# Kernel optimization log

Hardware: AMD Instinct MI355X
Metric: run time of the kernel (lower is better)

Reference implementation:

```python
import jax, jax.numpy as jnp
import numpy as np
from jax import lax

WINDOW_SIZE = 11
SIGMA = 1.5
MAX_VAL = 1.0
C1 = (0.01 * MAX_VAL) ** 2
C2 = (0.03 * MAX_VAL) ** 2
PAD = (WINDOW_SIZE - 1) // 2


def _gaussian_kernel2d(ksize: int, sigma: float) -> jnp.ndarray:
    x = jnp.arange(ksize, dtype=jnp.float32) - ksize // 2
    g = jnp.exp(-(x ** 2) / (2.0 * sigma ** 2))
    g = g / jnp.sum(g)
    return jnp.outer(g, g)  # [k, k]


def _filter2d(x: jnp.ndarray, kernel2d: jnp.ndarray) -> jnp.ndarray:
    # depthwise conv: x [B,C,H,W], kernel repeated per channel -> [C,1,k,k]
    c = x.shape[1]
    k = jnp.broadcast_to(kernel2d[None, None], (c, 1, WINDOW_SIZE, WINDOW_SIZE)).astype(x.dtype)
    return lax.conv_general_dilated(
        x, k,
        window_strides=(1, 1),
        padding=((PAD, PAD), (PAD, PAD)),
        dimension_numbers=("NCHW", "OIHW", "NCHW"),
        feature_group_count=c,
    )


def setup_inputs() -> dict:
    key = jax.random.key(0)
    k1, k2 = jax.random.split(key)
    img1 = jax.random.uniform(k1, (16, 3, 512, 512), dtype=jnp.float32)
    img2 = jax.random.uniform(k2, (16, 3, 512, 512), dtype=jnp.float32)
    return {"img1": img1, "img2": img2}


def reference(img1, img2):
    kernel = _gaussian_kernel2d(WINDOW_SIZE, SIGMA)
    mu1 = _filter2d(img1, kernel)
    mu2 = _filter2d(img2, kernel)
    mu1_sq = mu1 * mu1
    mu2_sq = mu2 * mu2
    mu1_mu2 = mu1 * mu2
    sigma1_sq = _filter2d(img1 * img1, kernel) - mu1_sq
    sigma2_sq = _filter2d(img2 * img2, kernel) - mu2_sq
    sigma12 = _filter2d(img1 * img2, kernel) - mu1_mu2
    ssim_map = ((2.0 * mu1_mu2 + C1) * (2.0 * sigma12 + C2)) / (
        (mu1_sq + mu2_sq + C1) * (sigma1_sq + sigma2_sq + C2)
    )
    loss = jnp.clip(1.0 - ssim_map, 0.0, 1.0) / 2.0
    return jnp.mean(loss)  # reduction='mean'
```

## Files before the change

### kernel.cpp

```cpp
#include <hip/hip_runtime.h>


#define BATCH  16
#define CHAN   3
#define H_     512
#define W_     512
#define HW     (H_ * W_)
#define CH_H   32
#define NSTEP  (CH_H + 10)
#define NPIX   ((long)BATCH*CHAN*H_*W_)

#define GW0 0.0010284f
#define GW1 0.0075988f
#define GW2 0.0360008f
#define GW3 0.1093554f
#define GW4 0.2130056f
#define GW5 0.2660117f

typedef float v2  __attribute__((ext_vector_type(2)));
typedef float v4f __attribute__((ext_vector_type(4)));

__device__ __forceinline__ float wg(int k) {
    return (k == 0 || k == 10) ? GW0
         : (k == 1 || k == 9)  ? GW1
         : (k == 2 || k == 8)  ? GW2
         : (k == 3 || k == 7)  ? GW3
         : (k == 4 || k == 6)  ? GW4 : GW5;
}

__device__ __forceinline__ v2 pfma(v2 a, v2 b, v2 c) {
#if __has_builtin(__builtin_elementwise_fma)
    return __builtin_elementwise_fma(a, b, c);
#else
    v2 r; r.x = fmaf(a.x, b.x, c.x); r.y = fmaf(a.y, b.y, c.y); return r;
#endif
}
__device__ __forceinline__ v2 psfma(float s, v2 b, v2 c) {
    v2 sv; sv.x = s; sv.y = s;
    return pfma(sv, b, c);
}

__device__ __forceinline__ float ssim_retire(float mu1, float mu2,
                                             float x11, float x22, float x12) {
    const float c1 = 1.0e-4f;
    const float c2 = 9.0e-4f;
    float mu1s = mu1 * mu1;
    float mu2s = mu2 * mu2;
    float m12  = mu1 * mu2;
    float num  = (2.0f * m12 + c1) * (2.0f * (x12 - m12) + c2);
    float den  = (mu1s + mu2s + c1) * ((x11 - mu1s) + (x22 - mu2s) + c2);
#if __has_builtin(__builtin_amdgcn_rcpf)
    float l = 1.0f - num * __builtin_amdgcn_rcpf(den);
#else
    float l = 1.0f - num / den;
#endif
    return fminf(fmaxf(l, 0.0f), 1.0f);
}

#define DECL(i) v2 P##i = {0.f, 0.f}, Q##i = {0.f, 0.f}; float E##i = 0.f
#define ACCI(i) do { const float wj_ = wg(10 - (i));             \
    P##i = psfma(wj_, hmm, P##i);                                \
    Q##i = psfma(wj_, hss, Q##i);                                \
    E##i = fmaf(wj_, hm12, E##i); } while (0)
#define SHIFT(i, j) P##i = P##j; Q##i = Q##j; E##i = E##j

__global__ __launch_bounds__(256) void ssim_kernel(const float* __restrict__ img1,
                                                   const float* __restrict__ img2,
                                                   float* __restrict__ out) {
    __shared__ __align__(16) v2 sp[4][2][80];
    __shared__ float wsum[4];

    const int tid  = threadIdx.x;
    const int lane = tid & 63;
    const int wv   = tid >> 6;

    const int wid   = blockIdx.x * 4 + wv;
    const int plane = wid >> 7;
    const int rem   = wid & 127;
    const int strip = rem & 7;
    const int chunk = rem >> 3;
    const int y0 = chunk * CH_H;
    const int c0 = strip * 64;

    const int  cg   = c0 - 6 + 2 * lane;
    const bool cok  = (cg >= 0) && (cg < W_) && (lane < 38);
    const int  cix  = cok ? cg : 0;
    const float msk = cok ? 1.0f : 0.0f;

    const size_t pb = (size_t)plane * HW;
    const float* __restrict__ p1 = img1 + pb;
    const float* __restrict__ p2 = img2 + pb;

    v2 (*st)[80] = sp[wv];

    DECL(0); DECL(1); DECL(2); DECL(3); DECL(4); DECL(5);
    DECL(6); DECL(7); DECL(8); DECL(9); DECL(10);
    float lsum = 0.0f;

    v2 cva = {0.f, 0.f}, cvb = {0.f, 0.f};
    {
        int r = y0 - 5;
        if ((unsigned)r < (unsigned)H_) {
            size_t off = (size_t)r * W_ + cix;
            v2 a = *(const v2*)(p1 + off);
            v2 b = *(const v2*)(p2 + off);
            cva = a * msk; cvb = b * msk;
        }
    }

#pragma unroll 1
    for (int sb = 0; sb < NSTEP / 2; ++sb) {
#pragma unroll
        for (int j = 0; j < 2; ++j) {
            const int step = sb * 2 + j;
            const int par  = j;

            if (lane < 38) {
                v4f w; w.x = cva.x; w.y = cvb.x; w.z = cva.y; w.w = cvb.y;
                *(v4f*)&st[par][2 * lane] = w;
            }
            __asm__ __volatile__("" ::: "memory");

            {
                int r = y0 + step - 4;
                cva = (v2){0.f, 0.f}; cvb = (v2){0.f, 0.f};
                if ((unsigned)r < (unsigned)H_) {
                    size_t off = (size_t)r * W_ + cix;
                    v2 a = *(const v2*)(p1 + off);
                    v2 b = *(const v2*)(p2 + off);
                    cva = a * msk; cvb = b * msk;
                }
            }

            v2 hmm = {0.f, 0.f}, hss = {0.f, 0.f};
            float hm12 = 0.f;
#pragma unroll
            for (int k = 0; k < 11; ++k) {
                v2 ab = st[par][lane + 1 + k];
                float wk = wg(k);
                v2 t = ab;
                t.x *= wk; t.y *= wk;
                hmm += t;
                hss = pfma(t, ab, hss);
                hm12 = fmaf(t.x, ab.y, hm12);
            }

            ACCI(0); ACCI(1); ACCI(2); ACCI(3); ACCI(4); ACCI(5);
            ACCI(6); ACCI(7); ACCI(8); ACCI(9); ACCI(10);

            if (step >= 10) lsum += ssim_retire(P0.x, P0.y, Q0.x, Q0.y, E0);

            SHIFT(0, 1); SHIFT(1, 2); SHIFT(2, 3); SHIFT(3, 4); SHIFT(4, 5);
            SHIFT(5, 6); SHIFT(6, 7); SHIFT(7, 8); SHIFT(8, 9); SHIFT(9, 10);
            P10 = (v2){0.f, 0.f}; Q10 = (v2){0.f, 0.f}; E10 = 0.f;
        }
    }

#pragma unroll
    for (int off = 32; off > 0; off >>= 1) lsum += __shfl_down(lsum, off);
    if (lane == 0) wsum[wv] = lsum;
    __syncthreads();
    if (tid == 0) {
        float bs = wsum[0] + wsum[1] + wsum[2] + wsum[3];
        atomicAdd(out, bs * (0.5f / (float)NPIX));
    }
}

extern "C" void kernel_launch(void* const* d_in, const int* in_sizes, int n_in,
                              void* d_out, int out_size, void* d_ws, size_t ws_size,
                              hipStream_t stream) {
    const float* img1 = (const float*)d_in[0];
    const float* img2 = (const float*)d_in[1];
    float* out = (float*)d_out;

    hipMemsetAsync(out, 0, sizeof(float), stream);

    ssim_kernel<<<dim3(8 * 16 * BATCH * CHAN / 4), 256, 0, stream>>>(img1, img2, out);
}
```

Baseline: 174.8 us.

## Double row chunk height, prefetch rows two ahead, and trim vertical accumulator

Each wave now covers 64 output rows instead of 32, which halves the grid and cuts the 10-row vertical halo overhead per wave. Global row loads are issued two steps ahead through a small register ring, giving each load more time to land. The first tap of the horizontal sum and the zero-init of the newest vertical accumulator are folded into direct assignments, dropping a few FMAs per step. The cost is fewer waves in flight (768 blocks total) and a few more live registers.

```diff
diff --git a/kernel.cpp b/kernel.cpp
--- a/kernel.cpp
+++ b/kernel.cpp
@@ -6,7 +6,7 @@
 #define H_     512
 #define W_     512
 #define HW     (H_ * W_)
-#define CH_H   32
+#define CH_H   64
 #define NSTEP  (CH_H + 10)
 #define NPIX   ((long)BATCH*CHAN*H_*W_)
 
@@ -64,6 +64,16 @@
     E##i = fmaf(wj_, hm12, E##i); } while (0)
 #define SHIFT(i, j) P##i = P##j; Q##i = Q##j; E##i = E##j
 
+#define LOADROW(r_, da_, db_) do {                                \
+    int r = (r_);                                                 \
+    da_ = (v2){0.f, 0.f}; db_ = (v2){0.f, 0.f};                   \
+    if ((unsigned)r < (unsigned)H_) {         \
+        size_t off = (size_t)r * W_ + cix;                        \
+        v2 a_ = *(const v2*)(p1 + off);                           \
+        v2 b_ = *(const v2*)(p2 + off);                           \
+        da_ = a_ * msk; db_ = b_ * msk;                           \
+    } } while (0)
+
 __global__ __launch_bounds__(256) void ssim_kernel(const float* __restrict__ img1,
                                                    const float* __restrict__ img2,
                                                    float* __restrict__ out) {
@@ -75,8 +85,8 @@
     const int wv   = tid >> 6;
 
     const int wid   = blockIdx.x * 4 + wv;
-    const int plane = wid >> 7;
-    const int rem   = wid & 127;
+    const int plane = wid >> 6;
+    const int rem   = wid & 63;
     const int strip = rem & 7;
     const int chunk = rem >> 3;
     const int y0 = chunk * CH_H;
@@ -97,16 +107,9 @@
     DECL(6); DECL(7); DECL(8); DECL(9); DECL(10);
     float lsum = 0.0f;
 
-    v2 cva = {0.f, 0.f}, cvb = {0.f, 0.f};
-    {
-        int r = y0 - 5;
-        if ((unsigned)r < (unsigned)H_) {
-            size_t off = (size_t)r * W_ + cix;
-            v2 a = *(const v2*)(p1 + off);
-            v2 b = *(const v2*)(p2 + off);
-            cva = a * msk; cvb = b * msk;
-        }
-    }
+    v2 r0a, r0b, r1a, r1b;
+    LOADROW(y0 - 5, r0a, r0b);
+    LOADROW(y0 - 4, r1a, r1b);
 
 #pragma unroll 1
     for (int sb = 0; sb < NSTEP / 2; ++sb) {
@@ -115,27 +118,21 @@
             const int step = sb * 2 + j;
             const int par  = j;
 
+            v2 r2a, r2b;
+            LOADROW(y0 + step - 3, r2a, r2b);
+
             if (lane < 38) {
-                v4f w; w.x = cva.x; w.y = cvb.x; w.z = cva.y; w.w = cvb.y;
+                v4f w; w.x = r0a.x; w.y = r0b.x; w.z = r0a.y; w.w = r0b.y;
                 *(v4f*)&st[par][2 * lane] = w;
             }
             __asm__ __volatile__("" ::: "memory");
 
-            {
-                int r = y0 + step - 4;
-                cva = (v2){0.f, 0.f}; cvb = (v2){0.f, 0.f};
-                if ((unsigned)r < (unsigned)H_) {
-                    size_t off = (size_t)r * W_ + cix;
-                    v2 a = *(const v2*)(p1 + off);
-                    v2 b = *(const v2*)(p2 + off);
-                    cva = a * msk; cvb = b * msk;
-                }
-            }
-
-            v2 hmm = {0.f, 0.f}, hss = {0.f, 0.f};
-            float hm12 = 0.f;
+            v2 ab0 = st[par][lane + 1];
+            v2 hmm = ab0 * wg(0);
+            v2 hss = hmm * ab0;
+            float hm12 = hmm.x * ab0.y;
 #pragma unroll
-            for (int k = 0; k < 11; ++k) {
+            for (int k = 1; k < 11; ++k) {
                 v2 ab = st[par][lane + 1 + k];
                 float wk = wg(k);
                 v2 t = ab;
@@ -145,14 +142,16 @@
                 hm12 = fmaf(t.x, ab.y, hm12);
             }
 
-            ACCI(0); ACCI(1); ACCI(2); ACCI(3); ACCI(4); ACCI(5);
-            ACCI(6); ACCI(7); ACCI(8); ACCI(9); ACCI(10);
+            ACCI(0); ACCI(1); ACCI(2); ACCI(3); ACCI(4);
+            ACCI(5); ACCI(6); ACCI(7); ACCI(8); ACCI(9);
 
             if (step >= 10) lsum += ssim_retire(P0.x, P0.y, Q0.x, Q0.y, E0);
 
             SHIFT(0, 1); SHIFT(1, 2); SHIFT(2, 3); SHIFT(3, 4); SHIFT(4, 5);
-            SHIFT(5, 6); SHIFT(6, 7); SHIFT(7, 8); SHIFT(8, 9); SHIFT(9, 10);
-            P10 = (v2){0.f, 0.f}; Q10 = (v2){0.f, 0.f}; E10 = 0.f;
+            SHIFT(5, 6); SHIFT(6, 7); SHIFT(7, 8); SHIFT(8, 9);
+            P9 = hmm * wg(0); Q9 = hss * wg(0); E9 = hm12 * wg(0);
+
+            r0a = r1a; r0b = r1b; r1a = r2a; r1b = r2b;
         }
     }
 
@@ -175,5 +174,5 @@
 
     hipMemsetAsync(out, 0, sizeof(float), stream);
 
-    ssim_kernel<<<dim3(8 * 16 * BATCH * CHAN / 4), 256, 0, stream>>>(img1, img2, out);
+    ssim_kernel<<<dim3(8 * 8 * BATCH * CHAN / 4), 256, 0, stream>>>(img1, img2, out);
 }
```

Measured after the change: 166.6 us. -4.6%, faster.

## Compute two output columns per lane with wider strips and vectorized LDS reads

Applied to the files above, without the earlier changes.

Each lane now produces two adjacent output columns, so a wave covers a 128-column strip and the grid shrinks by half. Every lane contributes to the staged row and six halo lanes load the extra border, which removes the old pattern where 26 of 64 lanes sat idle. Horizontal taps are read with wide v4 shared-memory loads and shared between the two columns, cutting LDS traffic and overhead per output. The cost is twice the vertical-accumulator registers, which may lower occupancy, and the double-buffered LDS staging is replaced by a single buffer relying on wave-local ordering.

```diff
diff --git a/kernel.cpp b/kernel.cpp
--- a/kernel.cpp
+++ b/kernel.cpp
@@ -57,17 +57,27 @@
     return fminf(fmaxf(l, 0.0f), 1.0f);
 }
 
-#define DECL(i) v2 P##i = {0.f, 0.f}, Q##i = {0.f, 0.f}; float E##i = 0.f
+#define DECL(i) v2 PA##i = {0.f,0.f}, QA##i = {0.f,0.f}, PB##i = {0.f,0.f}, \
+                   QB##i = {0.f,0.f}; float EA##i = 0.f, EB##i = 0.f
 #define ACCI(i) do { const float wj_ = wg(10 - (i));             \
-    P##i = psfma(wj_, hmm, P##i);                                \
-    Q##i = psfma(wj_, hss, Q##i);                                \
-    E##i = fmaf(wj_, hm12, E##i); } while (0)
-#define SHIFT(i, j) P##i = P##j; Q##i = Q##j; E##i = E##j
+    PA##i = psfma(wj_, hmmA, PA##i);                             \
+    QA##i = psfma(wj_, hssA, QA##i);                             \
+    EA##i = fmaf(wj_, hm12A, EA##i);                             \
+    PB##i = psfma(wj_, hmmB, PB##i);                             \
+    QB##i = psfma(wj_, hssB, QB##i);                             \
+    EB##i = fmaf(wj_, hm12B, EB##i); } while (0)
+#define SHIFT(i, j) PA##i = PA##j; QA##i = QA##j; EA##i = EA##j; \
+                    PB##i = PB##j; QB##i = QB##j; EB##i = EB##j
+
+#define HT_A(ab_, k_) { v2 t = (ab_) * wg(k_); hmmA += t; \
+    hssA = pfma(t, (ab_), hssA); hm12A = fmaf(t.x, (ab_).y, hm12A); }
+#define HT_B(ab_, k_) { v2 t = (ab_) * wg(k_); hmmB += t; \
+    hssB = pfma(t, (ab_), hssB); hm12B = fmaf(t.x, (ab_).y, hm12B); }
 
 __global__ __launch_bounds__(256) void ssim_kernel(const float* __restrict__ img1,
                                                    const float* __restrict__ img2,
                                                    float* __restrict__ out) {
-    __shared__ __align__(16) v2 sp[4][2][80];
+    __shared__ __align__(16) v2 sp[4][144];
     __shared__ float wsum[4];
 
     const int tid  = threadIdx.x;
@@ -75,85 +85,106 @@
     const int wv   = tid >> 6;
 
     const int wid   = blockIdx.x * 4 + wv;
-    const int plane = wid >> 7;
-    const int rem   = wid & 127;
-    const int strip = rem & 7;
-    const int chunk = rem >> 3;
+    const int plane = wid >> 6;
+    const int rem   = wid & 63;
+    const int strip = rem & 3;
+    const int chunk = rem >> 2;
     const int y0 = chunk * CH_H;
-    const int c0 = strip * 64;
+    const int c0 = strip * 128;
 
     const int  cg   = c0 - 6 + 2 * lane;
-    const bool cok  = (cg >= 0) && (cg < W_) && (lane < 38);
+    const bool cok  = (cg >= 0);
     const int  cix  = cok ? cg : 0;
     const float msk = cok ? 1.0f : 0.0f;
+    const int  hg   = c0 + 122 + 2 * lane;
+    const bool hok  = (lane < 6) && (hg + 1 < W_);
+    const int  hix  = hok ? hg : 0;
+    const float hmsk = hok ? 1.0f : 0.0f;
 
     const size_t pb = (size_t)plane * HW;
     const float* __restrict__ p1 = img1 + pb;
     const float* __restrict__ p2 = img2 + pb;
 
-    v2 (*st)[80] = sp[wv];
+    v2* st = sp[wv];
 
     DECL(0); DECL(1); DECL(2); DECL(3); DECL(4); DECL(5);
     DECL(6); DECL(7); DECL(8); DECL(9); DECL(10);
     float lsum = 0.0f;
 
-    v2 cva = {0.f, 0.f}, cvb = {0.f, 0.f};
+    v2 ma, mb, ha, hb;
     {
         int r = y0 - 5;
-        if ((unsigned)r < (unsigned)H_) {
-            size_t off = (size_t)r * W_ + cix;
-            v2 a = *(const v2*)(p1 + off);
-            v2 b = *(const v2*)(p2 + off);
-            cva = a * msk; cvb = b * msk;
+        bool rok = (unsigned)r < (unsigned)H_;
+        size_t off = (size_t)(rok ? r : 0) * W_;
+        float mm = rok ? msk : 0.0f, hm = rok ? hmsk : 0.0f;
+        ma = *(const v2*)(p1 + off + cix) * mm;
+        mb = *(const v2*)(p2 + off + cix) * mm;
+        ha = *(const v2*)(p1 + off + hix) * hm;
+        hb = *(const v2*)(p2 + off + hix) * hm;
+    }
+
+#pragma unroll 2
+    for (int step = 0; step < NSTEP; ++step) {
+        const int yy = step - 10;
+
+        {
+            v4f w; w.x = ma.x; w.y = mb.x; w.z = ma.y; w.w = mb.y;
+            *(v4f*)&st[2 * lane] = w;
+            if (lane < 6) {
+                v4f wh; wh.x = ha.x; wh.y = hb.x; wh.z = ha.y; wh.w = hb.y;
+                *(v4f*)&st[128 + 2 * lane] = wh;
+            }
         }
-    }
-
-#pragma unroll 1
-    for (int sb = 0; sb < NSTEP / 2; ++sb) {
-#pragma unroll
-        for (int j = 0; j < 2; ++j) {
-            const int step = sb * 2 + j;
-            const int par  = j;
-
-            if (lane < 38) {
-                v4f w; w.x = cva.x; w.y = cvb.x; w.z = cva.y; w.w = cvb.y;
-                *(v4f*)&st[par][2 * lane] = w;
-            }
-            __asm__ __volatile__("" ::: "memory");
-
-            {
-                int r = y0 + step - 4;
-                cva = (v2){0.f, 0.f}; cvb = (v2){0.f, 0.f};
-                if ((unsigned)r < (unsigned)H_) {
-                    size_t off = (size_t)r * W_ + cix;
-                    v2 a = *(const v2*)(p1 + off);
-                    v2 b = *(const v2*)(p2 + off);
-                    cva = a * msk; cvb = b * msk;
-                }
-            }
-
-            v2 hmm = {0.f, 0.f}, hss = {0.f, 0.f};
-            float hm12 = 0.f;
-#pragma unroll
-            for (int k = 0; k < 11; ++k) {
-                v2 ab = st[par][lane + 1 + k];
-                float wk = wg(k);
-                v2 t = ab;
-                t.x *= wk; t.y *= wk;
-                hmm += t;
-                hss = pfma(t, ab, hss);
-                hm12 = fmaf(t.x, ab.y, hm12);
-            }
-
-            ACCI(0); ACCI(1); ACCI(2); ACCI(3); ACCI(4); ACCI(5);
-            ACCI(6); ACCI(7); ACCI(8); ACCI(9); ACCI(10);
-
-            if (step >= 10) lsum += ssim_retire(P0.x, P0.y, Q0.x, Q0.y, E0);
-
-            SHIFT(0, 1); SHIFT(1, 2); SHIFT(2, 3); SHIFT(3, 4); SHIFT(4, 5);
-            SHIFT(5, 6); SHIFT(6, 7); SHIFT(7, 8); SHIFT(8, 9); SHIFT(9, 10);
-            P10 = (v2){0.f, 0.f}; Q10 = (v2){0.f, 0.f}; E10 = 0.f;
+        __asm__ __volatile__("" ::: "memory");
+
+        {
+            int r = y0 + step - 4;
+            bool rok = (unsigned)r < (unsigned)H_;
+            size_t off = (size_t)(rok ? r : 0) * W_;
+            float mm = rok ? msk : 0.0f, hm = rok ? hmsk : 0.0f;
+            ma = *(const v2*)(p1 + off + cix) * mm;
+            mb = *(const v2*)(p2 + off + cix) * mm;
+            ha = *(const v2*)(p1 + off + hix) * hm;
+            hb = *(const v2*)(p2 + off + hix) * hm;
         }
+
+        v2 m1  = st[2 * lane + 1];
+        v4f r1 = *(const v4f*)&st[2 * lane + 2];
+        v4f r2 = *(const v4f*)&st[2 * lane + 4];
+        v4f r3 = *(const v4f*)&st[2 * lane + 6];
+        v4f r4 = *(const v4f*)&st[2 * lane + 8];
+        v4f r5 = *(const v4f*)&st[2 * lane + 10];
+        v2 m12 = st[2 * lane + 12];
+        v2 m2  = {r1.x, r1.y}, m3  = {r1.z, r1.w};
+        v2 m4  = {r2.x, r2.y}, m5  = {r2.z, r2.w};
+        v2 m6  = {r3.x, r3.y}, m7  = {r3.z, r3.w};
+        v2 m8  = {r4.x, r4.y}, m9  = {r4.z, r4.w};
+        v2 m10 = {r5.x, r5.y}, m11 = {r5.z, r5.w};
+
+        v2 hmmA = m1 * wg(0);
+        v2 hssA = hmmA * m1;
+        float hm12A = hmmA.x * m1.y;
+        HT_A(m2, 1); HT_A(m3, 2); HT_A(m4, 3); HT_A(m5, 4); HT_A(m6, 5);
+        HT_A(m7, 6); HT_A(m8, 7); HT_A(m9, 8); HT_A(m10, 9); HT_A(m11, 10);
+        v2 hmmB = m2 * wg(0);
+        v2 hssB = hmmB * m2;
+        float hm12B = hmmB.x * m2.y;
+        HT_B(m3, 1); HT_B(m4, 2); HT_B(m5, 3); HT_B(m6, 4); HT_B(m7, 5);
+        HT_B(m8, 6); HT_B(m9, 7); HT_B(m10, 8); HT_B(m11, 9); HT_B(m12, 10);
+        __asm__ __volatile__("" ::: "memory");
+
+        ACCI(0); ACCI(1); ACCI(2); ACCI(3); ACCI(4); ACCI(5);
+        ACCI(6); ACCI(7); ACCI(8); ACCI(9); ACCI(10);
+
+        if (yy >= 0) {
+            lsum += ssim_retire(PA0.x, PA0.y, QA0.x, QA0.y, EA0);
+            lsum += ssim_retire(PB0.x, PB0.y, QB0.x, QB0.y, EB0);
+        }
+
+        SHIFT(0, 1); SHIFT(1, 2); SHIFT(2, 3); SHIFT(3, 4); SHIFT(4, 5);
+        SHIFT(5, 6); SHIFT(6, 7); SHIFT(7, 8); SHIFT(8, 9); SHIFT(9, 10);
+        PA10 = (v2){0.f, 0.f}; QA10 = (v2){0.f, 0.f}; EA10 = 0.f;
+        PB10 = (v2){0.f, 0.f}; QB10 = (v2){0.f, 0.f}; EB10 = 0.f;
     }
 
 #pragma unroll
@@ -175,5 +206,5 @@
 
     hipMemsetAsync(out, 0, sizeof(float), stream);
 
-    ssim_kernel<<<dim3(8 * 16 * BATCH * CHAN / 4), 256, 0, stream>>>(img1, img2, out);
-}
+    ssim_kernel<<<dim3(4 * 16 * BATCH * CHAN / 4), 256, 0, stream>>>(img1, img2, out);
+}
```

Result: faster. 157.0 us (-10.1%).
